# Performance work log

Measured on AMD Instinct MI355X. Metric: run time of the kernel, lower is better.

The kernel has to match this reference:

```python
import jax, jax.numpy as jnp
import numpy as np

B, T = 32, 4096
ATTN_DIM, ENC_DIM, DEC_DIM = 128, 512, 1024


def setup_inputs() -> dict:
    key = jax.random.key(0)
    k1, k2, k3, k4, k5, k6 = jax.random.split(key, 6)
    return {
        "query": jax.random.normal(k1, (B, DEC_DIM), dtype=jnp.float32),
        "memory": jax.random.normal(k2, (B, T, ENC_DIM), dtype=jnp.float32),
        "attention_weights_cum": jax.random.uniform(k3, (B, T), dtype=jnp.float32),
        "Wq": jax.random.normal(k4, (DEC_DIM, ATTN_DIM), dtype=jnp.float32) * (1.0 / np.sqrt(DEC_DIM)),
        "Wm": jax.random.normal(k5, (ENC_DIM, ATTN_DIM), dtype=jnp.float32) * (1.0 / np.sqrt(ENC_DIM)),
        "v": jax.random.normal(k6, (ATTN_DIM,), dtype=jnp.float32),
    }


def reference(query, memory, attention_weights_cum, Wq, Wm, v):
    # processed_query: [B, 1, A]; processed_memory: [B, T, A]
    pq = jnp.einsum('bd,da->ba', query, Wq)[:, None, :]
    pm = jnp.einsum('bte,ea->bta', memory, Wm)
    # scores: [B, T] = sum_a tanh(pq + pm) * v
    scores = jnp.einsum('bta,a->bt', jnp.tanh(pq + pm), v)
    alignments = jax.nn.softmax(scores, axis=-1)  # [B, T]
    context = jnp.einsum('bt,bte->be', alignments, memory)  # [B, E]
    return context, alignments
```

## Files before the change

### kernel.cpp

```cpp
#include <hip/hip_runtime.h>
#include <hip/hip_bf16.h>
#include <math.h>

#define B_SZ 32
#define T_SZ 4096
#define A_SZ 128
#define E_SZ 512
#define D_SZ 1024
#define NCH  32

typedef __attribute__((ext_vector_type(8))) short short8;
typedef __attribute__((ext_vector_type(4))) float f32x4;

static __device__ __forceinline__ unsigned short f32_to_bf16_rne(float x) {
    unsigned int u = __float_as_uint(x);
    unsigned int r = (u + 0x7fffu + ((u >> 16) & 1u)) >> 16;
    return (unsigned short)r;
}
static __device__ __forceinline__ float bf16_to_f32(unsigned short h) {
    return __uint_as_float(((unsigned int)h) << 16);
}
static __device__ __forceinline__ float tanh_fast(float x) {
    float ax = fabsf(x);
    float e  = __expf(2.f * ax);
    float r  = 1.f - 2.f / (e + 1.f);
    return __builtin_copysignf(r, x);
}

__global__ __launch_bounds__(256) void k_prep(const float* __restrict__ q,
                                              const float* __restrict__ Wq,
                                              const float* __restrict__ Wm,
                                              float* __restrict__ pq,
                                              unsigned short* __restrict__ WmTh,
                                              unsigned short* __restrict__ WmTl) {
    const int tid = threadIdx.x;
    if (blockIdx.x < 32) {
        const int b = blockIdx.x;
        __shared__ float ql[D_SZ];
        #pragma unroll
        for (int s = 0; s < D_SZ / 256; ++s)
            ql[s * 256 + tid] = q[b * D_SZ + s * 256 + tid];
        __syncthreads();
        if (tid < A_SZ) {
            const int a = tid;
            float acc = 0.f;
            #pragma unroll 8
            for (int d = 0; d < D_SZ; ++d)
                acc = fmaf(ql[d], Wq[d * A_SZ + a], acc);
            pq[b * A_SZ + a] = acc;
        }
    } else {
        const int a = blockIdx.x - 32;
        for (int e = tid; e < E_SZ; e += 256) {
            float x = Wm[(size_t)e * A_SZ + a];
            unsigned short h = f32_to_bf16_rne(x);
            float r = x - bf16_to_f32(h);
            unsigned short l = f32_to_bf16_rne(r);
            WmTh[(size_t)a * E_SZ + e] = h;
            WmTl[(size_t)a * E_SZ + e] = l;
        }
    }
}

#define AST 36
#define BST 40

__global__ __launch_bounds__(256, 4) void k_fused(
    const float* __restrict__ mem,
    const unsigned short* __restrict__ WmTh,
    const unsigned short* __restrict__ WmTl,
    const float* __restrict__ pq,
    const float* __restrict__ v,
    float* __restrict__ scores_raw,
    float* __restrict__ ctx_part,
    float* __restrict__ mZ)
{
    __shared__ unsigned short Ah[128 * AST];
    __shared__ unsigned short Al[128 * AST];
    __shared__ unsigned short Bh[128 * BST];
    __shared__ unsigned short Bl[128 * BST];
    __shared__ float sc[128];
    __shared__ float wbuf[128];
    __shared__ float red[8];

    const int cb = blockIdx.x;
    const int b  = blockIdx.y;
    const int t0 = cb * 128;
    const int tid = threadIdx.x;
    const int w = tid >> 6;
    const int lane = tid & 63;
    const int l16 = lane & 15;
    const int lk = lane >> 4;
    const int rot = (cb + b) & 15;

    const float* memB = mem + ((size_t)b * T_SZ + t0) * E_SZ;

    const int ar0 = tid >> 3;
    const int ae4 = (tid & 7) << 2;

    f32x4 acc[2][8];
    #pragma unroll
    for (int m = 0; m < 2; ++m)
        #pragma unroll
        for (int n = 0; n < 8; ++n)
            acc[m][n] = (f32x4){0.f, 0.f, 0.f, 0.f};

    float4 ra[4];
    {
        const int e0 = rot * 32;
        #pragma unroll
        for (int s = 0; s < 4; ++s)
            ra[s] = *(const float4*)(memB + (size_t)(ar0 + s * 32) * E_SZ + e0 + ae4);
    }

    for (int c = 0; c < 16; ++c) {
        const int cc = (c + rot) & 15;
        const int e0 = cc * 32;

        short8 rbh[2], rbl[2];
        #pragma unroll
        for (int s = 0; s < 2; ++s) {
            int idx = s * 256 + tid;
            int a   = idx >> 2;
            int es  = (idx & 3) << 3;
            rbh[s] = *(const short8*)&WmTh[(size_t)a * E_SZ + e0 + es];
            rbl[s] = *(const short8*)&WmTl[(size_t)a * E_SZ + e0 + es];
        }

        float4 rn[4];
        if (c < 15) {
            const int en = ((c + 1 + rot) & 15) * 32;
            #pragma unroll
            for (int s = 0; s < 4; ++s)
                rn[s] = *(const float4*)(memB + (size_t)(ar0 + s * 32) * E_SZ + en + ae4);
        }

        #pragma unroll
        for (int s = 0; s < 2; ++s) {
            int idx = s * 256 + tid;
            int a   = idx >> 2;
            int es  = (idx & 3) << 3;
            *(short8*)&Bh[a * BST + es] = rbh[s];
            *(short8*)&Bl[a * BST + es] = rbl[s];
        }

        #pragma unroll
        for (int s = 0; s < 4; ++s) {
            const int row = ar0 + s * 32;
            float xs[4] = {ra[s].x, ra[s].y, ra[s].z, ra[s].w};
            unsigned short h[4], l[4];
            #pragma unroll
            for (int k = 0; k < 4; ++k) {
                h[k] = f32_to_bf16_rne(xs[k]);
                l[k] = f32_to_bf16_rne(xs[k] - bf16_to_f32(h[k]));
            }
            unsigned int hp0 = (unsigned int)h[0] | ((unsigned int)h[1] << 16);
            unsigned int hp1 = (unsigned int)h[2] | ((unsigned int)h[3] << 16);
            unsigned int lp0 = (unsigned int)l[0] | ((unsigned int)l[1] << 16);
            unsigned int lp1 = (unsigned int)l[2] | ((unsigned int)l[3] << 16);
            *(uint2*)&Ah[row * AST + ae4] = make_uint2(hp0, hp1);
            *(uint2*)&Al[row * AST + ae4] = make_uint2(lp0, lp1);
        }
        __syncthreads();

        short8 ah[2], al[2];
        #pragma unroll
        for (int m = 0; m < 2; ++m) {
            int off = (w * 32 + m * 16 + l16) * AST + lk * 8;
            ah[m] = *(const short8*)&Ah[off];
            al[m] = *(const short8*)&Al[off];
        }
        #pragma unroll
        for (int n = 0; n < 8; ++n) {
            int boff = (n * 16 + l16) * BST + lk * 8;
            short8 bh = *(const short8*)&Bh[boff];
            short8 bl = *(const short8*)&Bl[boff];
            acc[0][n] = __builtin_amdgcn_mfma_f32_16x16x32_bf16(ah[0], bh, acc[0][n], 0, 0, 0);
            acc[1][n] = __builtin_amdgcn_mfma_f32_16x16x32_bf16(ah[1], bh, acc[1][n], 0, 0, 0);
            acc[0][n] = __builtin_amdgcn_mfma_f32_16x16x32_bf16(al[0], bh, acc[0][n], 0, 0, 0);
            acc[1][n] = __builtin_amdgcn_mfma_f32_16x16x32_bf16(al[1], bh, acc[1][n], 0, 0, 0);
            acc[0][n] = __builtin_amdgcn_mfma_f32_16x16x32_bf16(ah[0], bl, acc[0][n], 0, 0, 0);
            acc[1][n] = __builtin_amdgcn_mfma_f32_16x16x32_bf16(ah[1], bl, acc[1][n], 0, 0, 0);
        }
        __syncthreads();

        if (c < 15) {
            #pragma unroll
            for (int s = 0; s < 4; ++s) ra[s] = rn[s];
        }
    }

    float pqr[8], vr[8];
    #pragma unroll
    for (int n = 0; n < 8; ++n) {
        pqr[n] = pq[b * A_SZ + n * 16 + l16];
        vr[n]  = v[n * 16 + l16];
    }
    #pragma unroll
    for (int m = 0; m < 2; ++m) {
        float part[4] = {0.f, 0.f, 0.f, 0.f};
        #pragma unroll
        for (int n = 0; n < 8; ++n)
            #pragma unroll
            for (int r = 0; r < 4; ++r)
                part[r] += tanh_fast(pqr[n] + acc[m][n][r]) * vr[n];
        #pragma unroll
        for (int r = 0; r < 4; ++r) {
            #pragma unroll
            for (int off = 1; off < 16; off <<= 1)
                part[r] += __shfl_xor(part[r], off);
        }
        if (l16 == 0) {
            const int tl = w * 32 + m * 16 + lk * 4;
            #pragma unroll
            for (int r = 0; r < 4; ++r)
                sc[tl + r] = part[r];
        }
    }
    __syncthreads();

    float mv = sc[tid & 127];
    #pragma unroll
    for (int off = 1; off < 64; off <<= 1)
        mv = fmaxf(mv, __shfl_xor(mv, off));
    if (lane == 0) red[w] = mv;
    __syncthreads();
    const float Mc = fmaxf(fmaxf(red[0], red[1]), fmaxf(red[2], red[3]));

    float wv = 0.f;
    if (tid < 128) {
        wv = __expf(sc[tid] - Mc);
        wbuf[tid] = wv;
        scores_raw[(size_t)b * T_SZ + t0 + tid] = sc[tid];
    }
    float sv = wv;
    #pragma unroll
    for (int off = 1; off < 64; off <<= 1)
        sv += __shfl_xor(sv, off);
    if (lane == 0) red[4 + w] = sv;
    __syncthreads();
    if (tid == 0) {
        const float Zc = red[4] + red[5];
        mZ[(b * NCH + cb) * 2 + 0] = Mc;
        mZ[(b * NCH + cb) * 2 + 1] = Zc;
    }

    const int e2 = tid * 2;
    float2 a2 = make_float2(0.f, 0.f);
    #pragma unroll 8
    for (int t = 0; t < 128; ++t) {
        float2 mm = *(const float2*)(memB + (size_t)t * E_SZ + e2);
        const float wt = wbuf[t];
        a2.x = fmaf(wt, mm.x, a2.x);
        a2.y = fmaf(wt, mm.y, a2.y);
    }
    *(float2*)(ctx_part + ((size_t)cb * B_SZ + b) * E_SZ + e2) = a2;
}

__global__ __launch_bounds__(256) void k_combine(
    const float* __restrict__ ctx_part,
    const float* __restrict__ mZ,
    float* __restrict__ ctx,
    float* __restrict__ align)
{
    const int b = blockIdx.x;
    const int tid = threadIdx.x;
    float mc[NCH], zc[NCH], ec[NCH];
    float M = -1e30f;
    #pragma unroll
    for (int c = 0; c < NCH; ++c) {
        float2 p = *(const float2*)(mZ + (b * NCH + c) * 2);
        mc[c] = p.x; zc[c] = p.y;
        M = fmaxf(M, p.x);
    }
    float Z = 0.f;
    #pragma unroll
    for (int c = 0; c < NCH; ++c) {
        ec[c] = __expf(mc[c] - M);
        Z = fmaf(zc[c], ec[c], Z);
    }
    const float invZ = 1.f / Z;

    const int e2 = tid * 2;
    float2 a2 = make_float2(0.f, 0.f);
    #pragma unroll
    for (int c = 0; c < NCH; ++c) {
        float2 p = *(const float2*)(ctx_part + ((size_t)c * B_SZ + b) * E_SZ + e2);
        a2.x = fmaf(p.x, ec[c], a2.x);
        a2.y = fmaf(p.y, ec[c], a2.y);
    }
    float2 outv = make_float2(a2.x * invZ, a2.y * invZ);
    *(float2*)(ctx + (size_t)b * E_SZ + e2) = outv;

    float* row = align + (size_t)b * T_SZ;
    #pragma unroll
    for (int s = 0; s < 4; ++s) {
        float4 vv = *(float4*)&row[(s * 256 + tid) * 4];
        vv.x = __expf(vv.x - M) * invZ;
        vv.y = __expf(vv.y - M) * invZ;
        vv.z = __expf(vv.z - M) * invZ;
        vv.w = __expf(vv.w - M) * invZ;
        *(float4*)&row[(s * 256 + tid) * 4] = vv;
    }
}

extern "C" void kernel_launch(void* const* d_in, const int* in_sizes, int n_in,
                              void* d_out, int out_size, void* d_ws, size_t ws_size,
                              hipStream_t stream) {
    const float* query  = (const float*)d_in[0];
    const float* memory = (const float*)d_in[1];
    const float* Wq     = (const float*)d_in[3];
    const float* Wm     = (const float*)d_in[4];
    const float* v      = (const float*)d_in[5];

    float* ctx_out   = (float*)d_out;
    float* align_out = (float*)d_out + B_SZ * E_SZ;

    char* ws = (char*)d_ws;
    float*          pq       = (float*)(ws + 0);
    unsigned short* WmTh     = (unsigned short*)(ws + 16384);
    unsigned short* WmTl     = (unsigned short*)(ws + 147456);
    float*          mZ       = (float*)(ws + 278528);
    float*          ctx_part = (float*)(ws + 286720);

    k_prep<<<160, 256, 0, stream>>>(query, Wq, Wm, pq, WmTh, WmTl);
    k_fused<<<dim3(NCH, B_SZ), 256, 0, stream>>>(memory, WmTh, WmTl, pq, v,
                                                 align_out, ctx_part, mZ);
    k_combine<<<B_SZ, 256, 0, stream>>>(ctx_part, mZ, ctx_out, align_out);
}
```

Measured before the change: 468.3 us.

## Load memory A-fragments directly to registers and double-buffer Wm tiles

The kernel no longer stages the memory tile through LDS. Each lane loads the fp32 values it needs for its MFMA A-fragment straight into registers and splits them into bf16 hi/lo by truncation instead of round-to-nearest. The Wm B tiles are double-buffered in LDS so one barrier per chunk suffices, and the occupancy hint drops from 4 to 3 blocks per SM. This removes the A-tile LDS writes and reads plus one sync per chunk, at the cost of less coalesced 32-byte-per-lane global reads and a slightly different hi/lo split.

```diff
diff --git a/kernel.cpp b/kernel.cpp
--- a/kernel.cpp
+++ b/kernel.cpp
@@ -11,6 +11,9 @@
 
 typedef __attribute__((ext_vector_type(8))) short short8;
 typedef __attribute__((ext_vector_type(4))) float f32x4;
+typedef __attribute__((ext_vector_type(4))) unsigned int u32x4;
+
+union cvt8 { u32x4 u; short8 s; };
 
 static __device__ __forceinline__ unsigned short f32_to_bf16_rne(float x) {
     unsigned int u = __float_as_uint(x);
@@ -25,6 +28,22 @@
     float e  = __expf(2.f * ax);
     float r  = 1.f - 2.f / (e + 1.f);
     return __builtin_copysignf(r, x);
+}
+
+static __device__ __forceinline__ void split8(const float4 x0, const float4 x1,
+                                              short8& hi, short8& lo) {
+    float xs[8] = {x0.x, x0.y, x0.z, x0.w, x1.x, x1.y, x1.z, x1.w};
+    cvt8 h, l;
+    #pragma unroll
+    for (int j = 0; j < 4; ++j) {
+        unsigned int u0 = __float_as_uint(xs[2 * j]);
+        unsigned int u1 = __float_as_uint(xs[2 * j + 1]);
+        h.u[j] = (u0 >> 16) | (u1 & 0xffff0000u);
+        float lo0 = xs[2 * j]     - __uint_as_float(u0 & 0xffff0000u);
+        float lo1 = xs[2 * j + 1] - __uint_as_float(u1 & 0xffff0000u);
+        l.u[j] = (__float_as_uint(lo0) >> 16) | (__float_as_uint(lo1) & 0xffff0000u);
+    }
+    hi = h.s; lo = l.s;
 }
 
 __global__ __launch_bounds__(256) void k_prep(const float* __restrict__ q,
@@ -62,10 +81,9 @@
     }
 }
 
-#define AST 36
 #define BST 40
 
-__global__ __launch_bounds__(256, 4) void k_fused(
+__global__ __launch_bounds__(256, 3) void k_fused(
     const float* __restrict__ mem,
     const unsigned short* __restrict__ WmTh,
     const unsigned short* __restrict__ WmTl,
@@ -75,10 +93,8 @@
     float* __restrict__ ctx_part,
     float* __restrict__ mZ)
 {
-    __shared__ unsigned short Ah[128 * AST];
-    __shared__ unsigned short Al[128 * AST];
-    __shared__ unsigned short Bh[128 * BST];
-    __shared__ unsigned short Bl[128 * BST];
+    __shared__ unsigned short Bh[2][128 * BST];
+    __shared__ unsigned short Bl[2][128 * BST];
     __shared__ float sc[128];
     __shared__ float wbuf[128];
     __shared__ float red[8];
@@ -95,8 +111,11 @@
 
     const float* memB = mem + ((size_t)b * T_SZ + t0) * E_SZ;
 
-    const int ar0 = tid >> 3;
-    const int ae4 = (tid & 7) << 2;
+    const int sa0 = tid >> 2;
+    const int ses = (tid & 3) << 3;
+
+    const int arow0 = w * 32 + l16;
+    const int acol  = lk * 8;
 
     f32x4 acc[2][8];
     #pragma unroll
@@ -105,76 +124,58 @@
         for (int n = 0; n < 8; ++n)
             acc[m][n] = (f32x4){0.f, 0.f, 0.f, 0.f};
 
-    float4 ra[4];
     {
         const int e0 = rot * 32;
         #pragma unroll
-        for (int s = 0; s < 4; ++s)
-            ra[s] = *(const float4*)(memB + (size_t)(ar0 + s * 32) * E_SZ + e0 + ae4);
-    }
+        for (int s = 0; s < 2; ++s) {
+            int a = sa0 + s * 64;
+            *(short8*)&Bh[0][a * BST + ses] = *(const short8*)&WmTh[(size_t)a * E_SZ + e0 + ses];
+            *(short8*)&Bl[0][a * BST + ses] = *(const short8*)&WmTl[(size_t)a * E_SZ + e0 + ses];
+        }
+    }
+    float4 rA[2][2];
+    {
+        const int e0 = rot * 32;
+        #pragma unroll
+        for (int m = 0; m < 2; ++m) {
+            const float* p = memB + (size_t)(arow0 + m * 16) * E_SZ + e0 + acol;
+            rA[m][0] = *(const float4*)p;
+            rA[m][1] = *(const float4*)(p + 4);
+        }
+    }
+    __syncthreads();
 
     for (int c = 0; c < 16; ++c) {
-        const int cc = (c + rot) & 15;
-        const int e0 = cc * 32;
+        const int cur = c & 1;
 
         short8 rbh[2], rbl[2];
-        #pragma unroll
-        for (int s = 0; s < 2; ++s) {
-            int idx = s * 256 + tid;
-            int a   = idx >> 2;
-            int es  = (idx & 3) << 3;
-            rbh[s] = *(const short8*)&WmTh[(size_t)a * E_SZ + e0 + es];
-            rbl[s] = *(const short8*)&WmTl[(size_t)a * E_SZ + e0 + es];
-        }
-
-        float4 rn[4];
+        float4 rn[2][2];
         if (c < 15) {
             const int en = ((c + 1 + rot) & 15) * 32;
             #pragma unroll
-            for (int s = 0; s < 4; ++s)
-                rn[s] = *(const float4*)(memB + (size_t)(ar0 + s * 32) * E_SZ + en + ae4);
-        }
-
-        #pragma unroll
-        for (int s = 0; s < 2; ++s) {
-            int idx = s * 256 + tid;
-            int a   = idx >> 2;
-            int es  = (idx & 3) << 3;
-            *(short8*)&Bh[a * BST + es] = rbh[s];
-            *(short8*)&Bl[a * BST + es] = rbl[s];
-        }
-
-        #pragma unroll
-        for (int s = 0; s < 4; ++s) {
-            const int row = ar0 + s * 32;
-            float xs[4] = {ra[s].x, ra[s].y, ra[s].z, ra[s].w};
-            unsigned short h[4], l[4];
-            #pragma unroll
-            for (int k = 0; k < 4; ++k) {
-                h[k] = f32_to_bf16_rne(xs[k]);
-                l[k] = f32_to_bf16_rne(xs[k] - bf16_to_f32(h[k]));
+            for (int s = 0; s < 2; ++s) {
+                int a = sa0 + s * 64;
+                rbh[s] = *(const short8*)&WmTh[(size_t)a * E_SZ + en + ses];
+                rbl[s] = *(const short8*)&WmTl[(size_t)a * E_SZ + en + ses];
             }
-            unsigned int hp0 = (unsigned int)h[0] | ((unsigned int)h[1] << 16);
-            unsigned int hp1 = (unsigned int)h[2] | ((unsigned int)h[3] << 16);
-            unsigned int lp0 = (unsigned int)l[0] | ((unsigned int)l[1] << 16);
-            unsigned int lp1 = (unsigned int)l[2] | ((unsigned int)l[3] << 16);
-            *(uint2*)&Ah[row * AST + ae4] = make_uint2(hp0, hp1);
-            *(uint2*)&Al[row * AST + ae4] = make_uint2(lp0, lp1);
-        }
-        __syncthreads();
+            #pragma unroll
+            for (int m = 0; m < 2; ++m) {
+                const float* p = memB + (size_t)(arow0 + m * 16) * E_SZ + en + acol;
+                rn[m][0] = *(const float4*)p;
+                rn[m][1] = *(const float4*)(p + 4);
+            }
+        }
 
         short8 ah[2], al[2];
         #pragma unroll
-        for (int m = 0; m < 2; ++m) {
-            int off = (w * 32 + m * 16 + l16) * AST + lk * 8;
-            ah[m] = *(const short8*)&Ah[off];
-            al[m] = *(const short8*)&Al[off];
-        }
+        for (int m = 0; m < 2; ++m)
+            split8(rA[m][0], rA[m][1], ah[m], al[m]);
+
         #pragma unroll
         for (int n = 0; n < 8; ++n) {
             int boff = (n * 16 + l16) * BST + lk * 8;
-            short8 bh = *(const short8*)&Bh[boff];
-            short8 bl = *(const short8*)&Bl[boff];
+            short8 bh = *(const short8*)&Bh[cur][boff];
+            short8 bl = *(const short8*)&Bl[cur][boff];
             acc[0][n] = __builtin_amdgcn_mfma_f32_16x16x32_bf16(ah[0], bh, acc[0][n], 0, 0, 0);
             acc[1][n] = __builtin_amdgcn_mfma_f32_16x16x32_bf16(ah[1], bh, acc[1][n], 0, 0, 0);
             acc[0][n] = __builtin_amdgcn_mfma_f32_16x16x32_bf16(al[0], bh, acc[0][n], 0, 0, 0);
@@ -182,12 +183,21 @@
             acc[0][n] = __builtin_amdgcn_mfma_f32_16x16x32_bf16(ah[0], bl, acc[0][n], 0, 0, 0);
             acc[1][n] = __builtin_amdgcn_mfma_f32_16x16x32_bf16(ah[1], bl, acc[1][n], 0, 0, 0);
         }
+
+        if (c < 15) {
+            #pragma unroll
+            for (int s = 0; s < 2; ++s) {
+                int a = sa0 + s * 64;
+                *(short8*)&Bh[cur ^ 1][a * BST + ses] = rbh[s];
+                *(short8*)&Bl[cur ^ 1][a * BST + ses] = rbl[s];
+            }
+            #pragma unroll
+            for (int m = 0; m < 2; ++m) {
+                rA[m][0] = rn[m][0];
+                rA[m][1] = rn[m][1];
+            }
+        }
         __syncthreads();
-
-        if (c < 15) {
-            #pragma unroll
-            for (int s = 0; s < 4; ++s) ra[s] = rn[s];
-        }
     }
 
     float pqr[8], vr[8];
```

Result: slower. 489.3 us (+4.5%).
